# Performance work log

Hardware: AMD Instinct MI355X
Metric: run time of the kernel (lower is better)

The kernel has to match this reference:

```python
import jax, jax.numpy as jnp
import numpy as np
from jax.scipy import special

B, N, DIM, H, DK, DV, F = 2, 1536, 1536, 8, 64, 64, 192


def _pos_embed(seq_len, feat):
    """Enformer relative positional basis: [2*seq_len-1, feat]."""
    per = feat // 6  # 3 basis families x (symmetric, antisymmetric)
    d = jnp.arange(-seq_len + 1, seq_len, dtype=jnp.float32)
    ad = jnp.abs(d)[:, None]  # [2N-1, 1]
    # exponential decay, log-spaced half lives
    half_life = 2.0 ** jnp.linspace(3.0, float(np.log2(seq_len)), per)
    expo = jnp.exp(-jnp.log(2.0) / half_life * ad)
    # central binary mask
    widths = 2.0 ** jnp.arange(1, per + 1, dtype=jnp.float32) - 1.0
    cmask = (widths > ad).astype(jnp.float32)
    # gamma pdf basis
    stddev = seq_len / (2.0 * per)
    start_mean = seq_len / per
    mean = jnp.linspace(start_mean, float(seq_len), per)
    conc = (mean / stddev) ** 2
    rate = mean / stddev ** 2
    log_unnorm = special.xlogy(conc - 1.0, ad) - rate * ad
    log_norm = special.gammaln(conc) - conc * jnp.log(rate)
    probs = jnp.exp(log_unnorm - log_norm) + 1e-8
    gamma = probs / jnp.max(probs, axis=-1, keepdims=True)
    emb = jnp.concatenate([expo, cmask, gamma], axis=-1)
    emb = jnp.concatenate([emb, jnp.sign(d)[:, None] * emb], axis=-1)
    return emb.astype(jnp.float32)


def _relative_shift(x):
    # x: [B, H, N, 2N-1] -> [B, H, N, N] (Transformer-XL shift)
    b, h, t1, t2 = x.shape
    x = jnp.pad(x, ((0, 0), (0, 0), (0, 0), (1, 0)))  # [B,H,N,2N]
    x = x.reshape(b, h, t2 + 1, t1)[:, :, 1:, :].reshape(b, h, t1, t2)
    return x[..., : (t2 + 2) // 2]


def setup_inputs() -> dict:
    key = jax.random.key(0)
    ks = jax.random.split(key, 8)
    s = 0.02
    return {
        "x": jax.random.normal(ks[0], (B, N, DIM), dtype=jnp.float32),
        "Wq": jax.random.normal(ks[1], (DIM, H * DK), dtype=jnp.float32) * s,
        "Wk": jax.random.normal(ks[2], (DIM, H * DK), dtype=jnp.float32) * s,
        "Wv": jax.random.normal(ks[3], (DIM, H * DV), dtype=jnp.float32) * s,
        "Wrel": jax.random.normal(ks[4], (F, H * DK), dtype=jnp.float32) * s,
        "Wout": jax.random.normal(ks[5], (H * DV, DIM), dtype=jnp.float32) * s,
        "bout": jnp.zeros((DIM,), dtype=jnp.float32),
        "rel_content_bias": jax.random.normal(ks[6], (1, H, 1, DK), dtype=jnp.float32),
        "rel_pos_bias": jax.random.normal(ks[7], (1, H, 1, DK), dtype=jnp.float32),
        "pos_embed": _pos_embed(N, F),  # [2N-1, F] buffer
    }


def reference(x, Wq, Wk, Wv, Wrel, Wout, bout, rel_content_bias, rel_pos_bias, pos_embed):
    b, n, _ = x.shape
    h, dk = rel_content_bias.shape[1], rel_content_bias.shape[3]
    dv = Wv.shape[1] // h
    scale = dk ** -0.5
    q = (x @ Wq).reshape(b, n, h, dk).transpose(0, 2, 1, 3) * scale  # [b,h,n,dk]
    k = (x @ Wk).reshape(b, n, h, dk).transpose(0, 2, 1, 3)
    v = (x @ Wv).reshape(b, n, h, dv).transpose(0, 2, 1, 3)
    content_logits = jnp.einsum('bhid,bhjd->bhij', q + rel_content_bias, k)
    rel_k = (pos_embed @ Wrel).reshape(-1, h, dk).transpose(1, 0, 2)  # [h,2n-1,dk]
    rel_logits = jnp.einsum('bhid,hjd->bhij', q + rel_pos_bias, rel_k)  # [b,h,n,2n-1]
    rel_logits = _relative_shift(rel_logits)  # [b,h,n,n]
    attn = jax.nn.softmax(content_logits + rel_logits, axis=-1)
    out = jnp.einsum('bhij,bhjd->bhid', attn, v)
    out = out.transpose(0, 2, 1, 3).reshape(b, n, h * dv)
    return out @ Wout + bout
```

## Files before the change

### kernel.cpp

```cpp
#include <hip/hip_runtime.h>

#define NSEQ  1536
#define HEADS 8
#define NREL  3071
#define NRELP 3072

typedef __bf16 bf16;
typedef __bf16 bf16x8 __attribute__((ext_vector_type(8)));
typedef __bf16 bf16x4 __attribute__((ext_vector_type(4)));
typedef float  f32x4  __attribute__((ext_vector_type(4)));

static __device__ __forceinline__ f32x4 mfma16(bf16x8 a, bf16x8 b, f32x4 c) {
  return __builtin_amdgcn_mfma_f32_16x16x32_bf16(a, b, c, 0, 0, 0);
}

static __device__ __forceinline__ void gload_lds16(const bf16* g, bf16* l) {
  __builtin_amdgcn_global_load_lds((const __attribute__((address_space(1))) void*)g,
                                   (__attribute__((address_space(3))) void*)l, 16, 0, 0);
}

#define DPP_F(v, ctrl) __int_as_float(__builtin_amdgcn_update_dpp(0, __float_as_int(v), ctrl, 0xF, 0xF, true))
static __device__ __forceinline__ float rowsum16(float v) {
  v += DPP_F(v, 0xB1);
  v += DPP_F(v, 0x4E);
  v += DPP_F(v, 0x124);
  v += DPP_F(v, 0x128);
  return v;
}

__global__ __launch_bounds__(256) void prep(const float* __restrict__ x, const float* __restrict__ pos,
                                            const float* __restrict__ Wq, const float* __restrict__ Wk,
                                            const float* __restrict__ Wv, const float* __restrict__ Wout,
                                            const float* __restrict__ Wrel,
                                            bf16* __restrict__ xb, bf16* __restrict__ posb,
                                            bf16* __restrict__ WT, bf16* __restrict__ WoT,
                                            bf16* __restrict__ WrT) {
  int blk = blockIdx.x;
  if (blk < 4608) {
    int i = blk * 256 + threadIdx.x;
    float4 v = ((const float4*)x)[i];
    bf16x4 o;
    o[0] = (bf16)v.x; o[1] = (bf16)v.y; o[2] = (bf16)v.z; o[3] = (bf16)v.w;
    ((bf16x4*)xb)[i] = o;
    return;
  }
  blk -= 4608;
  if (blk < 576) {
    int i = blk * 256 + threadIdx.x;
    if (i < (NREL * 192 / 4)) {
      float4 v = ((const float4*)pos)[i];
      bf16x4 o;
      o[0] = (bf16)v.x; o[1] = (bf16)v.y; o[2] = (bf16)v.z; o[3] = (bf16)v.w;
      ((bf16x4*)posb)[i] = o;
    }
    return;
  }
  blk -= 576;
  const float* in; bf16* out; int C, ostride, orowoff, cx, ry;
  if (blk < 768)       { in = Wq;   out = WT;  C = 512;  ostride = 1536; orowoff = 0;    cx = blk % 16; ry = blk / 16; }
  else if (blk < 1536) { blk -= 768;  in = Wk;   out = WT;  C = 512;  ostride = 1536; orowoff = 512;  cx = blk % 16; ry = blk / 16; }
  else if (blk < 2304) { blk -= 1536; in = Wv;   out = WT;  C = 512;  ostride = 1536; orowoff = 1024; cx = blk % 16; ry = blk / 16; }
  else if (blk < 3072) { blk -= 2304; in = Wout; out = WoT; C = 1536; ostride = 512;  orowoff = 0;    cx = blk % 48; ry = blk / 48; }
  else                 { blk -= 3072; in = Wrel; out = WrT; C = 512;  ostride = 192;  orowoff = 0;    cx = blk % 16; ry = blk / 16; }
  __shared__ float t[32][33];
  int tx = threadIdx.x & 31, ty = threadIdx.x >> 5;
  int r0 = ry * 32, c0 = cx * 32;
#pragma unroll
  for (int i = 0; i < 4; i++)
    t[ty + 8 * i][tx] = in[(size_t)(r0 + ty + 8 * i) * C + c0 + tx];
  __syncthreads();
#pragma unroll
  for (int i = 0; i < 4; i++)
    out[(size_t)(c0 + ty + 8 * i + orowoff) * ostride + r0 + tx] = (bf16)t[tx][ty + 8 * i];
}

static __device__ __forceinline__ void gemm_core(const bf16* __restrict__ A, const bf16* __restrict__ BT,
                                                 int Klen, int ldk, int m0, int n0, int M,
                                                 bf16* sa, bf16* sb, f32x4 acc[4][2]) {
  int tid = threadIdx.x, wave = tid >> 6, lane = tid & 63;
  int l15 = lane & 15, quad = lane >> 4;
  int lrow = lane >> 3, lcg = lane & 7;
  for (int k0 = 0; k0 < Klen; k0 += 64) {
    __syncthreads();
#pragma unroll
    for (int t = 0; t < 2; t++) {
      int row = wave * 16 + t * 8 + lrow;
      int ra = m0 + row; if (ra > M - 1) ra = M - 1;
      gload_lds16(A + (size_t)ra * ldk + k0 + ((lcg ^ (row & 7)) * 8), sa + (wave * 16 + t * 8) * 64);
    }
#pragma unroll
    for (int t = 0; t < 4; t++) {
      int row = wave * 32 + t * 8 + lrow;
      gload_lds16(BT + (size_t)(n0 + row) * ldk + k0 + ((lcg ^ (row & 7)) * 8), sb + (wave * 32 + t * 8) * 64);
    }
    __syncthreads();
#pragma unroll
    for (int kq = 0; kq < 2; kq++) {
      bf16x8 af[4], bfr[2];
#pragma unroll
      for (int rt = 0; rt < 4; rt++) {
        int row = rt * 16 + l15;
        af[rt] = *(const bf16x8*)&sa[row * 64 + (((kq * 4 + quad) ^ (row & 7)) * 8)];
      }
#pragma unroll
      for (int ct = 0; ct < 2; ct++) {
        int row = wave * 32 + ct * 16 + l15;
        bfr[ct] = *(const bf16x8*)&sb[row * 64 + (((kq * 4 + quad) ^ (row & 7)) * 8)];
      }
#pragma unroll
      for (int ct = 0; ct < 2; ct++)
#pragma unroll
        for (int rt = 0; rt < 4; rt++)
          acc[rt][ct] = mfma16(af[rt], bfr[ct], acc[rt][ct]);
    }
  }
}

__global__ __launch_bounds__(256) void gemm_qkv(const bf16* __restrict__ xb, const bf16* __restrict__ WT,
                                                const float* __restrict__ cb, const float* __restrict__ pb,
                                                bf16* __restrict__ qc, bf16* __restrict__ qp,
                                                bf16* __restrict__ kb, bf16* __restrict__ vt) {
  __shared__ __align__(16) bf16 sa[64 * 64];
  __shared__ __align__(16) bf16 sb[128 * 64];
  __shared__ __align__(16) bf16 tv[64 * 130];
  int tid = threadIdx.x, wave = tid >> 6, lane = tid & 63;
  int l15 = lane & 15, quad = lane >> 4;
  int m0 = blockIdx.x * 64, n0 = blockIdx.y * 128;
  f32x4 acc[4][2] = {};
  gemm_core(xb, WT, 1536, 1536, m0, n0, 3072, sa, sb, acc);
  int b = m0 / NSEQ, nseq0 = m0 % NSEQ;
  if (blockIdx.y < 8) {
    bool isq = blockIdx.y < 4;
#pragma unroll
    for (int rt = 0; rt < 4; rt++)
#pragma unroll
      for (int ct = 0; ct < 2; ct++)
#pragma unroll
        for (int r = 0; r < 4; r++) {
          int row = nseq0 + rt * 16 + quad * 4 + r;
          int colg = n0 + wave * 32 + ct * 16 + l15;
          int col = colg & 511;
          int h = col >> 6, d = col & 63;
          size_t o = ((size_t)(b * 8 + h) * NSEQ + row) * 64 + d;
          float v = acc[rt][ct][r];
          if (isq) {
            float qv = v * 0.125f;
            qc[o] = (bf16)(qv + cb[col]);
            qp[o] = (bf16)(qv + pb[col]);
          } else {
            kb[o] = (bf16)v;
          }
        }
  } else {
#pragma unroll
    for (int rt = 0; rt < 4; rt++)
#pragma unroll
      for (int ct = 0; ct < 2; ct++)
#pragma unroll
        for (int r = 0; r < 4; r++)
          tv[(rt * 16 + quad * 4 + r) * 130 + wave * 32 + ct * 16 + l15] = (bf16)acc[rt][ct][r];
    __syncthreads();
    int n = tid & 63, c0v = tid >> 6;
    int hbase = (blockIdx.y - 8) * 2;
#pragma unroll
    for (int hh = 0; hh < 2; hh++)
#pragma unroll
      for (int i = 0; i < 16; i++) {
        int dv = i * 4 + c0v;
        vt[((size_t)(b * 8 + hbase + hh) * 64 + dv) * NSEQ + nseq0 + n] = tv[n * 130 + hh * 64 + dv];
      }
  }
}

__global__ __launch_bounds__(256) void gemm_rel(const bf16* __restrict__ posb, const bf16* __restrict__ WrT,
                                                bf16* __restrict__ rk) {
  __shared__ __align__(16) bf16 sa[64 * 64];
  __shared__ __align__(16) bf16 sb[128 * 64];
  int tid = threadIdx.x, wave = tid >> 6, lane = tid & 63;
  int l15 = lane & 15, quad = lane >> 4;
  int m0 = blockIdx.x * 64, n0 = blockIdx.y * 128;
  f32x4 acc[4][2] = {};
  gemm_core(posb, WrT, 192, 192, m0, n0, NREL, sa, sb, acc);
#pragma unroll
  for (int rt = 0; rt < 4; rt++)
#pragma unroll
    for (int ct = 0; ct < 2; ct++)
#pragma unroll
      for (int r = 0; r < 4; r++) {
        int row = m0 + rt * 16 + quad * 4 + r;
        if (row < NREL) {
          int col = n0 + wave * 32 + ct * 16 + l15;
          rk[((size_t)(col >> 6) * NRELP + row) * 64 + (col & 63)] = (bf16)acc[rt][ct][r];
        }
      }
}

__global__ __launch_bounds__(256) void gemm_out(const bf16* __restrict__ A, const bf16* __restrict__ BT,
                                                float* __restrict__ C, const float* __restrict__ bias) {
  __shared__ __align__(16) bf16 sa[64 * 64];
  __shared__ __align__(16) bf16 sb[128 * 64];
  int tid = threadIdx.x, wave = tid >> 6, lane = tid & 63;
  int l15 = lane & 15, quad = lane >> 4;
  int m0 = blockIdx.x * 64, n0 = blockIdx.y * 128;
  f32x4 acc[4][2] = {};
  gemm_core(A, BT, 512, 512, m0, n0, 3072, sa, sb, acc);
#pragma unroll
  for (int rt = 0; rt < 4; rt++)
#pragma unroll
    for (int ct = 0; ct < 2; ct++)
#pragma unroll
      for (int r = 0; r < 4; r++) {
        int row = m0 + rt * 16 + quad * 4 + r;
        int col = n0 + wave * 32 + ct * 16 + l15;
        C[(size_t)row * 1536 + col] = acc[rt][ct][r] + bias[col];
      }
}

__global__ __launch_bounds__(256, 4) void attn(const bf16* __restrict__ qc, const bf16* __restrict__ qp,
                                               const bf16* __restrict__ kb, const bf16* __restrict__ vt,
                                               const bf16* __restrict__ rk,
                                               float* __restrict__ Opart, float* __restrict__ mlp) {
  __shared__ __align__(16) bf16 sk[64 * 64];
  __shared__ __align__(16) bf16 sv[64 * 64];
  __shared__ __align__(16) bf16 srel[128 * 64];
  __shared__ __align__(16) bf16 pls[4][16 * 72];
  int qb = blockIdx.x, bh = blockIdx.y, kz = blockIdx.z;
  int h = bh & 7;
  int i0 = qb * 64;
  int wave = threadIdx.x >> 6, lane = threadIdx.x & 63;
  int l15 = lane & 15, quad = lane >> 4;
  int lrow = lane >> 3, lcg = lane & 7;
  const bf16* qcb = qc + (size_t)bh * NSEQ * 64;
  const bf16* qpb = qp + (size_t)bh * NSEQ * 64;
  const bf16* kbb = kb + (size_t)bh * NSEQ * 64;
  const bf16* vtb = vt + (size_t)bh * 64 * NSEQ;
  const bf16* rkh = rk + (size_t)h * NRELP * 64;
  bf16* plsw = pls[wave];

  int qrow = i0 + wave * 16 + l15;
  bf16x8 aqc0 = *(const bf16x8*)(qcb + (size_t)qrow * 64 + quad * 8);
  bf16x8 aqc1 = *(const bf16x8*)(qcb + (size_t)qrow * 64 + 32 + quad * 8);
  bf16x8 aqp0 = *(const bf16x8*)(qpb + (size_t)qrow * 64 + quad * 8);
  bf16x8 aqp1 = *(const bf16x8*)(qpb + (size_t)qrow * 64 + 32 + quad * 8);

  int bidx[4];
  bool hisel[4];
#pragma unroll
  for (int r = 0; r < 4; r++) {
    int rl = quad * 4 + r;
    bidx[r] = (quad * 16 + ((l15 + 15 - rl) & 15)) << 2;
    hisel[r] = l15 > rl;
  }

  f32x4 acco[4] = {};
  float li[4] = {0.0f, 0.0f, 0.0f, 0.0f};

  int locbase = (3 - wave) * 16;
  for (int jt = 0; jt < 12; jt++) {
    int j0 = kz * 768 + jt * 64;
    int Rbase = 1472 + j0 - i0;
    __syncthreads();
#pragma unroll
    for (int t = 0; t < 2; t++) {
      int row = wave * 16 + t * 8 + lrow;
      gload_lds16(kbb + (size_t)(j0 + row) * 64 + ((lcg ^ (row & 7)) * 8),
                  sk + (wave * 16 + t * 8) * 64);
    }
#pragma unroll
    for (int t = 0; t < 2; t++) {
      int row = wave * 16 + t * 8 + lrow;
      gload_lds16(vtb + (size_t)row * NSEQ + j0 + ((lcg ^ (row & 7)) * 8),
                  sv + (wave * 16 + t * 8) * 64);
    }
#pragma unroll
    for (int t = 0; t < 4; t++) {
      int loc = wave * 32 + t * 8 + lrow;
      gload_lds16(rkh + (size_t)(Rbase + loc) * 64 + ((lcg ^ (loc & 7)) * 8),
                  srel + (wave * 32 + t * 8) * 64);
    }
    __syncthreads();
    f32x4 s[4] = {};
#pragma unroll
    for (int c = 0; c < 4; c++) {
      int key = c * 16 + l15;
      bf16x8 b0 = *(const bf16x8*)&sk[key * 64 + ((quad ^ (key & 7)) * 8)];
      bf16x8 b1 = *(const bf16x8*)&sk[key * 64 + (((4 + quad) ^ (key & 7)) * 8)];
      s[c] = mfma16(aqc0, b0, s[c]);
      s[c] = mfma16(aqc1, b1, s[c]);
    }
    f32x4 sb5[5];
#pragma unroll
    for (int cc = 0; cc < 5; cc++) {
      int loc = locbase + cc * 16 + l15;
      bf16x8 b0 = *(const bf16x8*)&srel[loc * 64 + ((quad ^ (loc & 7)) * 8)];
      bf16x8 b1 = *(const bf16x8*)&srel[loc * 64 + (((4 + quad) ^ (loc & 7)) * 8)];
      f32x4 z = {};
      z = mfma16(aqp0, b0, z);
      sb5[cc] = mfma16(aqp1, b1, z);
    }
#pragma unroll
    for (int r = 0; r < 4; r++) {
      float bp[5];
#pragma unroll
      for (int cc = 0; cc < 5; cc++)
        bp[cc] = __int_as_float(__builtin_amdgcn_ds_bpermute(bidx[r], __float_as_int(sb5[cc][r])));
#pragma unroll
      for (int c = 0; c < 4; c++)
        s[c][r] += hisel[r] ? bp[c + 1] : bp[c];
    }
#pragma unroll
    for (int c = 0; c < 4; c++)
#pragma unroll
      for (int r = 0; r < 4; r++) {
        float p = __expf(s[c][r] - 8.0f);
        bf16 pbh = (bf16)p;
        li[r] += (float)pbh;
        plsw[(quad * 4 + r) * 72 + c * 16 + l15] = pbh;
      }
#pragma unroll
    for (int ks = 0; ks < 2; ks++) {
      bf16x8 ap = *(const bf16x8*)&plsw[l15 * 72 + ks * 32 + quad * 8];
#pragma unroll
      for (int c = 0; c < 4; c++) {
        int dv = c * 16 + l15;
        bf16x8 bv = *(const bf16x8*)&sv[dv * 64 + (((ks * 4 + quad) ^ (dv & 7)) * 8)];
        acco[c] = mfma16(ap, bv, acco[c]);
      }
    }
  }
#pragma unroll
  for (int r = 0; r < 4; r++)
    li[r] = rowsum16(li[r]);
  int qt16 = qb * 4 + wave;
  size_t pbase = ((size_t)(bh * 96 + qt16) * 2 + kz);
#pragma unroll
  for (int c = 0; c < 4; c++)
#pragma unroll
    for (int r = 0; r < 4; r++)
      Opart[pbase * 1024 + (quad * 4 + r) * 64 + c * 16 + l15] = acco[c][r];
  if (l15 == 0) {
#pragma unroll
    for (int r = 0; r < 4; r++)
      mlp[pbase * 16 + quad * 4 + r] = li[r];
  }
}

__global__ void attn_merge(const float* __restrict__ Opart, const float* __restrict__ mlp,
                           bf16* __restrict__ O) {
  int qt = blockIdx.x, bh = blockIdx.y;
  int b = bh >> 3, h = bh & 7;
  int col = threadIdx.x & 63, rg = threadIdx.x >> 6;
  size_t base = (size_t)(bh * 96 + qt) * 2;
#pragma unroll
  for (int rr = 0; rr < 4; rr++) {
    int row = rg * 4 + rr;
    float L = mlp[base * 16 + row] + mlp[(base + 1) * 16 + row];
    float v = Opart[base * 1024 + row * 64 + col] + Opart[(base + 1) * 1024 + row * 64 + col];
    O[((size_t)(b * NSEQ + qt * 16 + row) * 8 + h) * 64 + col] = (bf16)(v / L);
  }
}

extern "C" void kernel_launch(void* const* d_in, const int* in_sizes, int n_in,
                              void* d_out, int out_size, void* d_ws, size_t ws_size,
                              hipStream_t stream) {
  const float* x    = (const float*)d_in[0];
  const float* Wq   = (const float*)d_in[1];
  const float* Wk   = (const float*)d_in[2];
  const float* Wv   = (const float*)d_in[3];
  const float* Wrel = (const float*)d_in[4];
  const float* Wout = (const float*)d_in[5];
  const float* bout = (const float*)d_in[6];
  const float* cb   = (const float*)d_in[7];
  const float* pb   = (const float*)d_in[8];
  const float* pos  = (const float*)d_in[9];
  float* out = (float*)d_out;

  char* ws = (char*)d_ws;
  size_t off = 0;
  auto alloc = [&](size_t bytes) {
    char* p = ws + off;
    off = (off + bytes + 255) & ~(size_t)255;
    return p;
  };
  bf16*  xb    = (bf16*)alloc(3072UL * 1536 * 2);
  bf16*  WT    = (bf16*)alloc(1536UL * 1536 * 2);
  bf16*  WoT   = (bf16*)alloc(1536UL * 512 * 2);
  bf16*  WrT   = (bf16*)alloc(512UL * 192 * 2);
  bf16*  posb  = (bf16*)alloc((size_t)NREL * 192 * 2);
  bf16*  qcb   = (bf16*)alloc(16UL * NSEQ * 64 * 2);
  bf16*  qpb   = (bf16*)alloc(16UL * NSEQ * 64 * 2);
  bf16*  kbb   = (bf16*)alloc(16UL * NSEQ * 64 * 2);
  bf16*  vtb   = (bf16*)alloc(16UL * NSEQ * 64 * 2);
  bf16*  rkb   = (bf16*)alloc(8UL * NRELP * 64 * 2);
  bf16*  Ob    = (bf16*)alloc(3072UL * 512 * 2);
  float* Opart = (float*)alloc(16UL * 96 * 2 * 1024 * 4);
  float* mlpw  = (float*)alloc(16UL * 96 * 2 * 16 * 4);

  prep<<<dim3(8352), 256, 0, stream>>>(x, pos, Wq, Wk, Wv, Wout, Wrel, xb, posb, WT, WoT, WrT);
  gemm_qkv<<<dim3(48, 12), 256, 0, stream>>>(xb, WT, cb, pb, qcb, qpb, kbb, vtb);
  gemm_rel<<<dim3(48, 4), 256, 0, stream>>>(posb, WrT, rkb);
  attn<<<dim3(24, 16, 2), 256, 0, stream>>>(qcb, qpb, kbb, vtb, rkb, Opart, mlpw);
  attn_merge<<<dim3(96, 16), 256, 0, stream>>>(Opart, mlpw, Ob);
  gemm_out<<<dim3(48, 12), 256, 0, stream>>>(Ob, WoT, out, bout);
}
```

Measured before the change: 176.7 us.

## Fuse rel GEMM into QKV GEMM, split attention KZ=4, merge in-kernel via atomics

Merges the positional-key GEMM into the QKV projection launch as extra grid rows, and raises the key-dimension split of attention from 2 to 4 so more blocks run in parallel. The separate merge kernel is removed: the last block per query tile, found with an atomic counter zeroed in prep, sums the partial outputs and writes the normalized bf16 result. Address arithmetic is hoisted out of the key loop and the P staging buffer reuses the relative-key shared tile, which frees LDS but adds a barrier. These cut launch count and improve occupancy, at the cost of more partial-sum traffic and fence/atomic overhead.

Result: slower. 397.0 us (+124.6%).

```diff
diff --git a/kernel.cpp b/kernel.cpp
--- a/kernel.cpp
+++ b/kernel.cpp
@@ -4,6 +4,7 @@
 #define HEADS 8
 #define NREL  3071
 #define NRELP 3072
+#define KZ    4
 
 typedef __bf16 bf16;
 typedef __bf16 bf16x8 __attribute__((ext_vector_type(8)));
@@ -34,7 +35,7 @@
                                             const float* __restrict__ Wrel,
                                             bf16* __restrict__ xb, bf16* __restrict__ posb,
                                             bf16* __restrict__ WT, bf16* __restrict__ WoT,
-                                            bf16* __restrict__ WrT) {
+                                            bf16* __restrict__ WrT, int* __restrict__ flags) {
   int blk = blockIdx.x;
   if (blk < 4608) {
     int i = blk * 256 + threadIdx.x;
@@ -56,6 +57,10 @@
     return;
   }
   blk -= 576;
+  if (blk >= 3168) {
+    for (int i = threadIdx.x; i < 384; i += 256) flags[i] = 0;
+    return;
+  }
   const float* in; bf16* out; int C, ostride, orowoff, cx, ry;
   if (blk < 768)       { in = Wq;   out = WT;  C = 512;  ostride = 1536; orowoff = 0;    cx = blk % 16; ry = blk / 16; }
   else if (blk < 1536) { blk -= 768;  in = Wk;   out = WT;  C = 512;  ostride = 1536; orowoff = 512;  cx = blk % 16; ry = blk / 16; }
@@ -116,17 +121,37 @@
   }
 }
 
-__global__ __launch_bounds__(256) void gemm_qkv(const bf16* __restrict__ xb, const bf16* __restrict__ WT,
-                                                const float* __restrict__ cb, const float* __restrict__ pb,
-                                                bf16* __restrict__ qc, bf16* __restrict__ qp,
-                                                bf16* __restrict__ kb, bf16* __restrict__ vt) {
+__global__ __launch_bounds__(256) void gemm_qkvrel(const bf16* __restrict__ xb, const bf16* __restrict__ WT,
+                                                   const bf16* __restrict__ posb, const bf16* __restrict__ WrT,
+                                                   const float* __restrict__ cb, const float* __restrict__ pb,
+                                                   bf16* __restrict__ qc, bf16* __restrict__ qp,
+                                                   bf16* __restrict__ kb, bf16* __restrict__ vt,
+                                                   bf16* __restrict__ rk) {
   __shared__ __align__(16) bf16 sa[64 * 64];
   __shared__ __align__(16) bf16 sb[128 * 64];
   __shared__ __align__(16) bf16 tv[64 * 130];
   int tid = threadIdx.x, wave = tid >> 6, lane = tid & 63;
   int l15 = lane & 15, quad = lane >> 4;
-  int m0 = blockIdx.x * 64, n0 = blockIdx.y * 128;
+  int m0 = blockIdx.x * 64;
   f32x4 acc[4][2] = {};
+  if (blockIdx.y >= 12) {
+    int n0 = (blockIdx.y - 12) * 128;
+    gemm_core(posb, WrT, 192, 192, m0, n0, NREL, sa, sb, acc);
+#pragma unroll
+    for (int rt = 0; rt < 4; rt++)
+#pragma unroll
+      for (int ct = 0; ct < 2; ct++)
+#pragma unroll
+        for (int r = 0; r < 4; r++) {
+          int row = m0 + rt * 16 + quad * 4 + r;
+          if (row < NREL) {
+            int col = n0 + wave * 32 + ct * 16 + l15;
+            rk[((size_t)(col >> 6) * NRELP + row) * 64 + (col & 63)] = (bf16)acc[rt][ct][r];
+          }
+        }
+    return;
+  }
+  int n0 = blockIdx.y * 128;
   gemm_core(xb, WT, 1536, 1536, m0, n0, 3072, sa, sb, acc);
   int b = m0 / NSEQ, nseq0 = m0 % NSEQ;
   if (blockIdx.y < 8) {
@@ -172,29 +197,6 @@
   }
 }
 
-__global__ __launch_bounds__(256) void gemm_rel(const bf16* __restrict__ posb, const bf16* __restrict__ WrT,
-                                                bf16* __restrict__ rk) {
-  __shared__ __align__(16) bf16 sa[64 * 64];
-  __shared__ __align__(16) bf16 sb[128 * 64];
-  int tid = threadIdx.x, wave = tid >> 6, lane = tid & 63;
-  int l15 = lane & 15, quad = lane >> 4;
-  int m0 = blockIdx.x * 64, n0 = blockIdx.y * 128;
-  f32x4 acc[4][2] = {};
-  gemm_core(posb, WrT, 192, 192, m0, n0, NREL, sa, sb, acc);
-#pragma unroll
-  for (int rt = 0; rt < 4; rt++)
-#pragma unroll
-    for (int ct = 0; ct < 2; ct++)
-#pragma unroll
-      for (int r = 0; r < 4; r++) {
-        int row = m0 + rt * 16 + quad * 4 + r;
-        if (row < NREL) {
-          int col = n0 + wave * 32 + ct * 16 + l15;
-          rk[((size_t)(col >> 6) * NRELP + row) * 64 + (col & 63)] = (bf16)acc[rt][ct][r];
-        }
-      }
-}
-
 __global__ __launch_bounds__(256) void gemm_out(const bf16* __restrict__ A, const bf16* __restrict__ BT,
                                                 float* __restrict__ C, const float* __restrict__ bias) {
   __shared__ __align__(16) bf16 sa[64 * 64];
@@ -219,11 +221,12 @@
 __global__ __launch_bounds__(256, 4) void attn(const bf16* __restrict__ qc, const bf16* __restrict__ qp,
                                                const bf16* __restrict__ kb, const bf16* __restrict__ vt,
                                                const bf16* __restrict__ rk,
-                                               float* __restrict__ Opart, float* __restrict__ mlp) {
+                                               float* __restrict__ Opart, float* __restrict__ mlp,
+                                               bf16* __restrict__ Ob, int* __restrict__ flags) {
   __shared__ __align__(16) bf16 sk[64 * 64];
   __shared__ __align__(16) bf16 sv[64 * 64];
   __shared__ __align__(16) bf16 srel[128 * 64];
-  __shared__ __align__(16) bf16 pls[4][16 * 72];
+  __shared__ int sflag;
   int qb = blockIdx.x, bh = blockIdx.y, kz = blockIdx.z;
   int h = bh & 7;
   int i0 = qb * 64;
@@ -232,10 +235,7 @@
   int lrow = lane >> 3, lcg = lane & 7;
   const bf16* qcb = qc + (size_t)bh * NSEQ * 64;
   const bf16* qpb = qp + (size_t)bh * NSEQ * 64;
-  const bf16* kbb = kb + (size_t)bh * NSEQ * 64;
-  const bf16* vtb = vt + (size_t)bh * 64 * NSEQ;
-  const bf16* rkh = rk + (size_t)h * NRELP * 64;
-  bf16* plsw = pls[wave];
+  bf16* plsw = srel + wave * (16 * 72);
 
   int qrow = i0 + wave * 16 + l15;
   bf16x8 aqc0 = *(const bf16x8*)(qcb + (size_t)qrow * 64 + quad * 8);
@@ -243,6 +243,38 @@
   bf16x8 aqp0 = *(const bf16x8*)(qpb + (size_t)qrow * 64 + quad * 8);
   bf16x8 aqp1 = *(const bf16x8*)(qpb + (size_t)qrow * 64 + 32 + quad * 8);
 
+  int swz0 = (quad ^ (l15 & 7)) * 8;
+  int swz1 = ((quad + 4) ^ (l15 & 7)) * 8;
+  int locbase = (3 - wave) * 16;
+  const bf16* pk0 = sk + l15 * 64 + swz0;
+  const bf16* pk1 = sk + l15 * 64 + swz1;
+  const bf16* pv0 = sv + l15 * 64 + swz0;
+  const bf16* pv1 = sv + l15 * 64 + swz1;
+  const bf16* pr0 = srel + (locbase + l15) * 64 + swz0;
+  const bf16* pr1 = srel + (locbase + l15) * 64 + swz1;
+  const bf16* plr = plsw + l15 * 72 + quad * 8;
+  bf16* plw = plsw + quad * 288 + l15;
+
+  int jbeg = kz * 384;
+  int Rbase0 = 1472 + jbeg - i0;
+  const bf16* kS[2]; const bf16* vS[2]; const bf16* rS[4];
+  bf16* kD[2]; bf16* vD[2]; bf16* rD[4];
+  int swzs = (lcg ^ lrow) * 8;
+#pragma unroll
+  for (int t = 0; t < 2; t++) {
+    int row = wave * 16 + t * 8 + lrow;
+    kS[t] = kb + (size_t)bh * NSEQ * 64 + (size_t)(jbeg + row) * 64 + swzs;
+    vS[t] = vt + (size_t)bh * 64 * NSEQ + (size_t)row * NSEQ + jbeg + swzs;
+    kD[t] = sk + (wave * 16 + t * 8) * 64;
+    vD[t] = sv + (wave * 16 + t * 8) * 64;
+  }
+#pragma unroll
+  for (int t = 0; t < 4; t++) {
+    int loc = wave * 32 + t * 8 + lrow;
+    rS[t] = rk + (size_t)h * NRELP * 64 + (size_t)(Rbase0 + loc) * 64 + swzs;
+    rD[t] = srel + (wave * 32 + t * 8) * 64;
+  }
+
   int bidx[4];
   bool hisel[4];
 #pragma unroll
@@ -255,49 +287,32 @@
   f32x4 acco[4] = {};
   float li[4] = {0.0f, 0.0f, 0.0f, 0.0f};
 
-  int locbase = (3 - wave) * 16;
-  for (int jt = 0; jt < 12; jt++) {
-    int j0 = kz * 768 + jt * 64;
-    int Rbase = 1472 + j0 - i0;
+  for (int jt = 0; jt < 6; jt++) {
     __syncthreads();
 #pragma unroll
     for (int t = 0; t < 2; t++) {
-      int row = wave * 16 + t * 8 + lrow;
-      gload_lds16(kbb + (size_t)(j0 + row) * 64 + ((lcg ^ (row & 7)) * 8),
-                  sk + (wave * 16 + t * 8) * 64);
-    }
-#pragma unroll
-    for (int t = 0; t < 2; t++) {
-      int row = wave * 16 + t * 8 + lrow;
-      gload_lds16(vtb + (size_t)row * NSEQ + j0 + ((lcg ^ (row & 7)) * 8),
-                  sv + (wave * 16 + t * 8) * 64);
+      gload_lds16(kS[t], kD[t]); kS[t] += 4096;
+      gload_lds16(vS[t], vD[t]); vS[t] += 64;
     }
 #pragma unroll
     for (int t = 0; t < 4; t++) {
-      int loc = wave * 32 + t * 8 + lrow;
-      gload_lds16(rkh + (size_t)(Rbase + loc) * 64 + ((lcg ^ (loc & 7)) * 8),
-                  srel + (wave * 32 + t * 8) * 64);
+      gload_lds16(rS[t], rD[t]); rS[t] += 4096;
     }
     __syncthreads();
     f32x4 s[4] = {};
 #pragma unroll
     for (int c = 0; c < 4; c++) {
-      int key = c * 16 + l15;
-      bf16x8 b0 = *(const bf16x8*)&sk[key * 64 + ((quad ^ (key & 7)) * 8)];
-      bf16x8 b1 = *(const bf16x8*)&sk[key * 64 + (((4 + quad) ^ (key & 7)) * 8)];
-      s[c] = mfma16(aqc0, b0, s[c]);
-      s[c] = mfma16(aqc1, b1, s[c]);
+      s[c] = mfma16(aqc0, *(const bf16x8*)(pk0 + c * 1024), s[c]);
+      s[c] = mfma16(aqc1, *(const bf16x8*)(pk1 + c * 1024), s[c]);
     }
     f32x4 sb5[5];
 #pragma unroll
     for (int cc = 0; cc < 5; cc++) {
-      int loc = locbase + cc * 16 + l15;
-      bf16x8 b0 = *(const bf16x8*)&srel[loc * 64 + ((quad ^ (loc & 7)) * 8)];
-      bf16x8 b1 = *(const bf16x8*)&srel[loc * 64 + (((4 + quad) ^ (loc & 7)) * 8)];
       f32x4 z = {};
-      z = mfma16(aqp0, b0, z);
-      sb5[cc] = mfma16(aqp1, b1, z);
-    }
+      z = mfma16(aqp0, *(const bf16x8*)(pr0 + cc * 1024), z);
+      sb5[cc] = mfma16(aqp1, *(const bf16x8*)(pr1 + cc * 1024), z);
+    }
+    __syncthreads();
 #pragma unroll
     for (int r = 0; r < 4; r++) {
       float bp[5];
@@ -315,15 +330,15 @@
         float p = __expf(s[c][r] - 8.0f);
         bf16 pbh = (bf16)p;
         li[r] += (float)pbh;
-        plsw[(quad * 4 + r) * 72 + c * 16 + l15] = pbh;
+        plw[r * 72 + c * 16] = pbh;
       }
 #pragma unroll
     for (int ks = 0; ks < 2; ks++) {
-      bf16x8 ap = *(const bf16x8*)&plsw[l15 * 72 + ks * 32 + quad * 8];
+      bf16x8 ap = *(const bf16x8*)(plr + ks * 32);
 #pragma unroll
       for (int c = 0; c < 4; c++) {
-        int dv = c * 16 + l15;
-        bf16x8 bv = *(const bf16x8*)&sv[dv * 64 + (((ks * 4 + quad) ^ (dv & 7)) * 8)];
+        const bf16* pvb = (ks == 0) ? pv0 : pv1;
+        bf16x8 bv = *(const bf16x8*)(pvb + c * 1024);
         acco[c] = mfma16(ap, bv, acco[c]);
       }
     }
@@ -332,7 +347,7 @@
   for (int r = 0; r < 4; r++)
     li[r] = rowsum16(li[r]);
   int qt16 = qb * 4 + wave;
-  size_t pbase = ((size_t)(bh * 96 + qt16) * 2 + kz);
+  size_t pbase = ((size_t)(bh * 96 + qt16)) * KZ + kz;
 #pragma unroll
   for (int c = 0; c < 4; c++)
 #pragma unroll
@@ -343,20 +358,39 @@
     for (int r = 0; r < 4; r++)
       mlp[pbase * 16 + quad * 4 + r] = li[r];
   }
-}
-
-__global__ void attn_merge(const float* __restrict__ Opart, const float* __restrict__ mlp,
-                           bf16* __restrict__ O) {
-  int qt = blockIdx.x, bh = blockIdx.y;
-  int b = bh >> 3, h = bh & 7;
-  int col = threadIdx.x & 63, rg = threadIdx.x >> 6;
-  size_t base = (size_t)(bh * 96 + qt) * 2;
-#pragma unroll
-  for (int rr = 0; rr < 4; rr++) {
-    int row = rg * 4 + rr;
-    float L = mlp[base * 16 + row] + mlp[(base + 1) * 16 + row];
-    float v = Opart[base * 1024 + row * 64 + col] + Opart[(base + 1) * 1024 + row * 64 + col];
-    O[((size_t)(b * NSEQ + qt * 16 + row) * 8 + h) * 64 + col] = (bf16)(v / L);
+  __threadfence();
+  __syncthreads();
+  if (threadIdx.x == 0) sflag = atomicAdd(&flags[bh * 24 + qb], 1);
+  __syncthreads();
+  if (sflag == KZ - 1) {
+    __threadfence();
+    int t = threadIdx.x;
+    int r = t >> 2, qo = (t & 3) * 16;
+    int qt = qb * 4 + (r >> 4), r16 = r & 15;
+    size_t ob = ((size_t)(bh * 96 + qt)) * KZ;
+    float L = 0.0f;
+    float o[16];
+#pragma unroll
+    for (int i = 0; i < 16; i++) o[i] = 0.0f;
+#pragma unroll
+    for (int z = 0; z < KZ; z++) {
+      L += mlp[(ob + z) * 16 + r16];
+      const float* P = Opart + (ob + z) * 1024 + r16 * 64 + qo;
+#pragma unroll
+      for (int i = 0; i < 4; i++) {
+        f32x4 v = ((const f32x4*)P)[i];
+#pragma unroll
+        for (int j = 0; j < 4; j++) o[i * 4 + j] += v[j];
+      }
+    }
+    float inv = 1.0f / L;
+    int b = bh >> 3;
+    bf16* dst = Ob + ((size_t)(b * NSEQ + i0 + r)) * 512 + h * 64 + qo;
+    bf16x8 w0, w1;
+#pragma unroll
+    for (int j = 0; j < 8; j++) { w0[j] = (bf16)(o[j] * inv); w1[j] = (bf16)(o[8 + j] * inv); }
+    ((bf16x8*)dst)[0] = w0;
+    ((bf16x8*)dst)[1] = w1;
   }
 }
 
@@ -393,13 +427,12 @@
   bf16*  vtb   = (bf16*)alloc(16UL * NSEQ * 64 * 2);
   bf16*  rkb   = (bf16*)alloc(8UL * NRELP * 64 * 2);
   bf16*  Ob    = (bf16*)alloc(3072UL * 512 * 2);
-  float* Opart = (float*)alloc(16UL * 96 * 2 * 1024 * 4);
-  float* mlpw  = (float*)alloc(16UL * 96 * 2 * 16 * 4);
-
-  prep<<<dim3(8352), 256, 0, stream>>>(x, pos, Wq, Wk, Wv, Wout, Wrel, xb, posb, WT, WoT, WrT);
-  gemm_qkv<<<dim3(48, 12), 256, 0, stream>>>(xb, WT, cb, pb, qcb, qpb, kbb, vtb);
-  gemm_rel<<<dim3(48, 4), 256, 0, stream>>>(posb, WrT, rkb);
-  attn<<<dim3(24, 16, 2), 256, 0, stream>>>(qcb, qpb, kbb, vtb, rkb, Opart, mlpw);
-  attn_merge<<<dim3(96, 16), 256, 0, stream>>>(Opart, mlpw, Ob);
+  float* Opart = (float*)alloc(16UL * 96 * KZ * 1024 * 4);
+  float* mlpw  = (float*)alloc(16UL * 96 * KZ * 16 * 4);
+  int*   flags = (int*)alloc(384 * 4);
+
+  prep<<<dim3(8353), 256, 0, stream>>>(x, pos, Wq, Wk, Wv, Wout, Wrel, xb, posb, WT, WoT, WrT, flags);
+  gemm_qkvrel<<<dim3(48, 16), 256, 0, stream>>>(xb, WT, posb, WrT, cb, pb, qcb, qpb, kbb, vtb, rkb);
+  attn<<<dim3(24, 16, KZ), 256, 0, stream>>>(qcb, qpb, kbb, vtb, rkb, Opart, mlpw, Ob, flags);
   gemm_out<<<dim3(48, 12), 256, 0, stream>>>(Ob, WoT, out, bout);
 }
```
